# Optimization experiments

Hardware: AMD Instinct MI355X
Metric: run time of the kernel (lower is better)

## Reference

```python
import jax, jax.numpy as jnp
import numpy as np

TEMPERATURE = 0.07
BASE_TEMPERATURE = 0.07
L_MAX = 16  # max number of session labels per dialogue
NEG_INF = -1e30


def setup_inputs() -> dict:
    key = jax.random.key(0)
    k1, k2, k3 = jax.random.split(key, 3)
    B, T, H = 128, 1024, 256
    features = jax.random.normal(k1, (B, T, H), dtype=jnp.float32)
    dialogue_lengths = jax.random.randint(k2, (B,), 1, T + 1)
    labels = jax.random.randint(k3, (B, T), 0, L_MAX)
    return {"features": features, "dialogue_lengths": dialogue_lengths, "labels": labels}


def reference(features, dialogue_lengths, labels):
    B, T, H = features.shape
    valid = jnp.arange(T)[None, :] < dialogue_lengths[:, None]            # [B,T]
    # one-hot label assignment, zeroed at padded positions
    oh = (labels[..., None] == jnp.arange(L_MAX)[None, None, :]) & valid[..., None]
    ohf = oh.astype(features.dtype)                                       # [B,T,L]
    counts = ohf.sum(axis=1)                                              # [B,L]
    # per-dialogue, per-label prototype = mean of member features
    proto_sum = jnp.einsum('btl,bth->blh', ohf, features)                 # [B,L,H]
    prototypes = proto_sum / jnp.maximum(counts, 1.0)[..., None]          # [B,L,H]
    # anchor-vs-prototype logits
    logits = jnp.einsum('bth,blh->btl', features, prototypes) / TEMPERATURE
    present = counts > 0                                                  # [B,L]
    logits = jnp.where(present[:, None, :], logits, NEG_INF)
    log_prob = jax.nn.log_softmax(logits, axis=-1)                        # [B,T,L]
    # mask is one-hot on each token's own label -> mean_log_prob_pos is log_prob at own label
    pos = jnp.take_along_axis(log_prob, labels[..., None], axis=-1)[..., 0]  # [B,T]
    tok_loss = -(TEMPERATURE / BASE_TEMPERATURE) * pos
    per_dialogue = jnp.sum(jnp.where(valid, tok_loss, 0.0), axis=1) / dialogue_lengths.astype(features.dtype)
    return per_dialogue.mean()
```

## Files before the change

kernel.cpp:

```cpp
#include <hip/hip_runtime.h>
#include <math.h>

#define B 128
#define T 1024
#define H 256
#define L 16
#define INV_TEMP (1.0f/0.07f)
#define NEG_INF -1e30f


__global__ __launch_bounds__(256) void proto_kernel(
    const float* __restrict__ feat, const int* __restrict__ dlen,
    const int* __restrict__ labels, float* __restrict__ ws_pp,
    int* __restrict__ ws_cntp) {
  __shared__ float acc[4][L * 128];
  __shared__ int labs[256];
  __shared__ int cnt[L];

  const int bx = blockIdx.x;
  const int b = bx >> 3;
  const int chunk = (bx >> 2) & 1;
  const int seg = bx & 3;
  const int tid = threadIdx.x;
  const int w = tid >> 6;
  const int lane = tid & 63;

  const int len = dlen[b];
  if (seg * 256 >= len) return;

  for (int i = tid; i < 4 * L * 128; i += 256) ((float*)acc)[i] = 0.f;
  labs[tid] = labels[(size_t)b * T + seg * 256 + tid];
  if (tid < L) cnt[tid] = 0;
  __syncthreads();

  if (chunk == 0 && (seg * 256 + tid) < len) atomicAdd(&cnt[labs[tid]], 1);

  int nt = len - seg * 256 - w * 64;
  if (nt > 64) nt = 64;
  const float2* fbase = (const float2*)(feat +
      ((size_t)b * T + seg * 256 + w * 64) * H + chunk * 128);
  float* a = acc[w];

  int j = 0;
  for (; j + 4 <= nt; j += 4) {
    float2 f0 = fbase[(size_t)(j + 0) * (H / 2) + lane];
    float2 f1 = fbase[(size_t)(j + 1) * (H / 2) + lane];
    float2 f2 = fbase[(size_t)(j + 2) * (H / 2) + lane];
    float2 f3 = fbase[(size_t)(j + 3) * (H / 2) + lane];
    const int l0 = labs[w * 64 + j + 0];
    const int l1 = labs[w * 64 + j + 1];
    const int l2 = labs[w * 64 + j + 2];
    const int l3 = labs[w * 64 + j + 3];
    float2* p0 = (float2*)&a[l0 * 128 + lane * 2];
    { float2 v = *p0; v.x += f0.x; v.y += f0.y; *p0 = v; }
    float2* p1 = (float2*)&a[l1 * 128 + lane * 2];
    { float2 v = *p1; v.x += f1.x; v.y += f1.y; *p1 = v; }
    float2* p2 = (float2*)&a[l2 * 128 + lane * 2];
    { float2 v = *p2; v.x += f2.x; v.y += f2.y; *p2 = v; }
    float2* p3 = (float2*)&a[l3 * 128 + lane * 2];
    { float2 v = *p3; v.x += f3.x; v.y += f3.y; *p3 = v; }
  }
  for (; j < nt; ++j) {
    float2 f = fbase[(size_t)j * (H / 2) + lane];
    const int lab = labs[w * 64 + j];
    float2* p = (float2*)&a[lab * 128 + lane * 2];
    float2 v = *p; v.x += f.x; v.y += f.y; *p = v;
  }
  __syncthreads();

  float* op = ws_pp + (((size_t)b * 4 + seg) * L) * H + chunk * 128;
  for (int e = tid; e < L * 128; e += 256) {
    const float s = acc[0][e] + acc[1][e] + acc[2][e] + acc[3][e];
    op[(e >> 7) * H + (e & 127)] = s;
  }
  if (chunk == 0 && tid < L) ws_cntp[(b * 4 + seg) * L + tid] = cnt[tid];
}

__global__ __launch_bounds__(256) void dots_kernel(
    const float* __restrict__ feat, const int* __restrict__ dlen,
    const float* __restrict__ ws_pp, const int* __restrict__ ws_cntp,
    float* __restrict__ ws_dots) {
  __shared__ float pr[L * 128];
  __shared__ int cnts[L];

  const int bx = blockIdx.x;
  const int b = bx >> 1;
  const int half = bx & 1;
  const int tid = threadIdx.x;

  const int len = dlen[b];
  const int nseg = (len + 255) >> 8;

  if (tid < L) {
    const int* cp = ws_cntp + b * 4 * L + tid;
    int c = 0;
    for (int s = 0; s < nseg; ++s) c += cp[s * L];
    cnts[tid] = c;
  }
  __syncthreads();

  const float* gp = ws_pp + ((size_t)b * 4 * L) * H + half * 128;
  for (int i = tid; i < L * 128; i += 256) {
    const int l = i >> 7, c = i & 127;
    float s = 0.f;
    for (int sg = 0; sg < nseg; ++sg) s += gp[(sg * L + l) * H + c];
    const int cn = cnts[l];
    pr[i] = s * (cn > 0 ? 1.f / (float)cn : 0.f);
  }
  __syncthreads();

  const float4* fv[4];
#pragma unroll
  for (int k = 0; k < 4; ++k) {
    const int t = k * 256 + tid;
    fv[k] = (const float4*)(feat + ((size_t)b * T + t) * H + half * 128);
  }

  float dot[4][L];
#pragma unroll
  for (int k = 0; k < 4; ++k)
#pragma unroll
    for (int l = 0; l < L; ++l) dot[k][l] = 0.f;

  for (int cb = 0; cb < 8; ++cb) {
    float4 f[4][4];
#pragma unroll
    for (int k = 0; k < 4; ++k) {
      if (k < nseg) {
#pragma unroll
        for (int q = 0; q < 4; ++q) f[k][q] = fv[k][cb * 4 + q];
      }
    }
#pragma unroll
    for (int q = 0; q < 4; ++q) {
#pragma unroll
      for (int l = 0; l < L; ++l) {
        const float4 p = *(const float4*)&pr[l * 128 + cb * 16 + q * 4];
#pragma unroll
        for (int k = 0; k < 4; ++k) {
          if (k < nseg) {
            dot[k][l] += f[k][q].x * p.x + f[k][q].y * p.y +
                         f[k][q].z * p.z + f[k][q].w * p.w;
          }
        }
      }
    }
  }

#pragma unroll
  for (int k = 0; k < 4; ++k) {
    const int t = k * 256 + tid;
    if (k < nseg && t < len) {
      float4* d = (float4*)(ws_dots + (((size_t)half * B + b) * T + t) * L);
#pragma unroll
      for (int q = 0; q < 4; ++q)
        d[q] = make_float4(dot[k][q * 4], dot[k][q * 4 + 1],
                           dot[k][q * 4 + 2], dot[k][q * 4 + 3]);
    }
  }
}

__global__ __launch_bounds__(256) void loss_kernel(
    const int* __restrict__ dlen, const int* __restrict__ labels,
    const int* __restrict__ ws_cntp, const float* __restrict__ ws_dots,
    float* __restrict__ out) {
  __shared__ int cnts[L];
  __shared__ float red[256];

  const int b = blockIdx.x >> 2;
  const int seg = blockIdx.x & 3;
  const int tid = threadIdx.x;

  const int len = dlen[b];
  if (seg * 256 >= len) return;
  const int nseg = (len + 255) >> 8;

  if (tid < L) {
    const int* cp = ws_cntp + b * 4 * L + tid;
    int c = 0;
    for (int s = 0; s < nseg; ++s) c += cp[s * L];
    cnts[tid] = c;
  }
  __syncthreads();

  const int t = seg * 256 + tid;
  float tok = 0.f;

  if (t < len) {
    const float* d0 = ws_dots + ((size_t)b * T + t) * L;
    const float* d1 = d0 + (size_t)B * T * L;
    float lg[L];
#pragma unroll
    for (int l = 0; l < L; ++l) {
      const float d = d0[l] + d1[l];
      lg[l] = (cnts[l] > 0) ? d * INV_TEMP : NEG_INF;
    }
    float m = lg[0];
#pragma unroll
    for (int l = 1; l < L; ++l) m = fmaxf(m, lg[l]);
    float se = 0.f;
#pragma unroll
    for (int l = 0; l < L; ++l) se += expf(lg[l] - m);
    const float lsp = m + logf(se);

    const int lab = labels[(size_t)b * T + t];
    float pos = 0.f;
#pragma unroll
    for (int l = 0; l < L; ++l) pos += (l == lab) ? lg[l] : 0.f;

    tok = lsp - pos;
  }

  red[tid] = tok;
  __syncthreads();
#pragma unroll
  for (int s = 128; s > 0; s >>= 1) {
    if (tid < s) red[tid] += red[tid + s];
    __syncthreads();
  }
  if (tid == 0) atomicAdd(out, red[0] / ((float)len * (float)B));
}

extern "C" void kernel_launch(void* const* d_in, const int* in_sizes, int n_in,
                              void* d_out, int out_size, void* d_ws, size_t ws_size,
                              hipStream_t stream) {
  const float* feat = (const float*)d_in[0];
  const int* dlen = (const int*)d_in[1];
  const int* labels = (const int*)d_in[2];
  float* out = (float*)d_out;

  float* ws_pp = (float*)d_ws;
  int* ws_cntp = (int*)(ws_pp + (size_t)B * 4 * L * H);
  float* ws_dots = (float*)(ws_cntp + (size_t)B * 4 * L);

  hipMemsetAsync(out, 0, sizeof(float), stream);
  proto_kernel<<<B * 8, 256, 0, stream>>>(feat, dlen, labels, ws_pp, ws_cntp);
  dots_kernel<<<B * 2, 256, 0, stream>>>(feat, dlen, ws_pp, ws_cntp, ws_dots);
  loss_kernel<<<B * 4, 256, 0, stream>>>(dlen, labels, ws_cntp, ws_dots, out);
}
```

Baseline: 226.3 us.

## Fuse dot-product and loss kernels, split tokens instead of hidden dim

The dots and loss kernels become one. Each block now holds the full 256-wide prototype set in shared memory and owns up to 512 tokens, so every thread has complete logits and computes the log-softmax loss in registers. This drops the dots workspace round trip, the cross-half reduction and one launch. Blocks past the dialogue length exit early. In exchange each block stages twice as much prototype data, and per-thread work grows with full-H dot products.

```diff
diff --git a/kernel.cpp b/kernel.cpp
--- a/kernel.cpp
+++ b/kernel.cpp
@@ -76,19 +76,21 @@
   if (chunk == 0 && tid < L) ws_cntp[(b * 4 + seg) * L + tid] = cnt[tid];
 }
 
-__global__ __launch_bounds__(256) void dots_kernel(
+__global__ __launch_bounds__(256) void dots_loss_kernel(
     const float* __restrict__ feat, const int* __restrict__ dlen,
-    const float* __restrict__ ws_pp, const int* __restrict__ ws_cntp,
-    float* __restrict__ ws_dots) {
-  __shared__ float pr[L * 128];
+    const int* __restrict__ labels, const float* __restrict__ ws_pp,
+    const int* __restrict__ ws_cntp, float* __restrict__ out) {
+  __shared__ float pr[L * H];
   __shared__ int cnts[L];
+  __shared__ float red[256];
 
   const int bx = blockIdx.x;
   const int b = bx >> 1;
-  const int half = bx & 1;
+  const int g = bx & 1;
   const int tid = threadIdx.x;
 
   const int len = dlen[b];
+  if (g * 512 >= len) return;
   const int nseg = (len + 255) >> 8;
 
   if (tid < L) {
@@ -99,9 +101,9 @@
   }
   __syncthreads();
 
-  const float* gp = ws_pp + ((size_t)b * 4 * L) * H + half * 128;
-  for (int i = tid; i < L * 128; i += 256) {
-    const int l = i >> 7, c = i & 127;
+  const float* gp = ws_pp + ((size_t)b * 4 * L) * H;
+  for (int i = tid; i < L * H; i += 256) {
+    const int l = i >> 8, c = i & 255;
     float s = 0.f;
     for (int sg = 0; sg < nseg; ++sg) s += gp[(sg * L + l) * H + c];
     const int cn = cnts[l];
@@ -109,92 +111,43 @@
   }
   __syncthreads();
 
-  const float4* fv[4];
-#pragma unroll
-  for (int k = 0; k < 4; ++k) {
-    const int t = k * 256 + tid;
-    fv[k] = (const float4*)(feat + ((size_t)b * T + t) * H + half * 128);
-  }
-
-  float dot[4][L];
-#pragma unroll
-  for (int k = 0; k < 4; ++k)
-#pragma unroll
-    for (int l = 0; l < L; ++l) dot[k][l] = 0.f;
-
-  for (int cb = 0; cb < 8; ++cb) {
-    float4 f[4][4];
-#pragma unroll
-    for (int k = 0; k < 4; ++k) {
-      if (k < nseg) {
-#pragma unroll
-        for (int q = 0; q < 4; ++q) f[k][q] = fv[k][cb * 4 + q];
+  const int t0 = g * 512 + tid;
+  const int t1 = t0 + 256;
+  const bool v1 = (g * 512 + 256) < len;
+  const float4* fv0 = (const float4*)(feat + ((size_t)b * T + t0) * H);
+  const float4* fv1 = (const float4*)(feat + ((size_t)b * T + t1) * H);
+
+  float dot0[L], dot1[L];
+#pragma unroll
+  for (int l = 0; l < L; ++l) { dot0[l] = 0.f; dot1[l] = 0.f; }
+
+#pragma unroll 2
+  for (int cb = 0; cb < 16; ++cb) {
+    float4 f0[4], f1[4];
+#pragma unroll
+    for (int q = 0; q < 4; ++q) f0[q] = fv0[cb * 4 + q];
+    if (v1) {
+#pragma unroll
+      for (int q = 0; q < 4; ++q) f1[q] = fv1[cb * 4 + q];
+    }
+#pragma unroll
+    for (int q = 0; q < 4; ++q) {
+#pragma unroll
+      for (int l = 0; l < L; ++l) {
+        const float4 p = *(const float4*)&pr[l * H + cb * 16 + q * 4];
+        dot0[l] += f0[q].x * p.x + f0[q].y * p.y + f0[q].z * p.z + f0[q].w * p.w;
+        if (v1)
+          dot1[l] += f1[q].x * p.x + f1[q].y * p.y + f1[q].z * p.z + f1[q].w * p.w;
       }
     }
-#pragma unroll
-    for (int q = 0; q < 4; ++q) {
-#pragma unroll
-      for (int l = 0; l < L; ++l) {
-        const float4 p = *(const float4*)&pr[l * 128 + cb * 16 + q * 4];
-#pragma unroll
-        for (int k = 0; k < 4; ++k) {
-          if (k < nseg) {
-            dot[k][l] += f[k][q].x * p.x + f[k][q].y * p.y +
-                         f[k][q].z * p.z + f[k][q].w * p.w;
-          }
-        }
-      }
-    }
-  }
-
-#pragma unroll
-  for (int k = 0; k < 4; ++k) {
-    const int t = k * 256 + tid;
-    if (k < nseg && t < len) {
-      float4* d = (float4*)(ws_dots + (((size_t)half * B + b) * T + t) * L);
-#pragma unroll
-      for (int q = 0; q < 4; ++q)
-        d[q] = make_float4(dot[k][q * 4], dot[k][q * 4 + 1],
-                           dot[k][q * 4 + 2], dot[k][q * 4 + 3]);
-    }
-  }
-}
-
-__global__ __launch_bounds__(256) void loss_kernel(
-    const int* __restrict__ dlen, const int* __restrict__ labels,
-    const int* __restrict__ ws_cntp, const float* __restrict__ ws_dots,
-    float* __restrict__ out) {
-  __shared__ int cnts[L];
-  __shared__ float red[256];
-
-  const int b = blockIdx.x >> 2;
-  const int seg = blockIdx.x & 3;
-  const int tid = threadIdx.x;
-
-  const int len = dlen[b];
-  if (seg * 256 >= len) return;
-  const int nseg = (len + 255) >> 8;
-
-  if (tid < L) {
-    const int* cp = ws_cntp + b * 4 * L + tid;
-    int c = 0;
-    for (int s = 0; s < nseg; ++s) c += cp[s * L];
-    cnts[tid] = c;
-  }
-  __syncthreads();
-
-  const int t = seg * 256 + tid;
+  }
+
   float tok = 0.f;
-
-  if (t < len) {
-    const float* d0 = ws_dots + ((size_t)b * T + t) * L;
-    const float* d1 = d0 + (size_t)B * T * L;
+  if (t0 < len) {
     float lg[L];
 #pragma unroll
-    for (int l = 0; l < L; ++l) {
-      const float d = d0[l] + d1[l];
-      lg[l] = (cnts[l] > 0) ? d * INV_TEMP : NEG_INF;
-    }
+    for (int l = 0; l < L; ++l)
+      lg[l] = (cnts[l] > 0) ? dot0[l] * INV_TEMP : NEG_INF;
     float m = lg[0];
 #pragma unroll
     for (int l = 1; l < L; ++l) m = fmaxf(m, lg[l]);
@@ -202,13 +155,29 @@
 #pragma unroll
     for (int l = 0; l < L; ++l) se += expf(lg[l] - m);
     const float lsp = m + logf(se);
-
-    const int lab = labels[(size_t)b * T + t];
+    const int lab = labels[(size_t)b * T + t0];
     float pos = 0.f;
 #pragma unroll
     for (int l = 0; l < L; ++l) pos += (l == lab) ? lg[l] : 0.f;
-
-    tok = lsp - pos;
+    tok += lsp - pos;
+  }
+  if (v1 && t1 < len) {
+    float lg[L];
+#pragma unroll
+    for (int l = 0; l < L; ++l)
+      lg[l] = (cnts[l] > 0) ? dot1[l] * INV_TEMP : NEG_INF;
+    float m = lg[0];
+#pragma unroll
+    for (int l = 1; l < L; ++l) m = fmaxf(m, lg[l]);
+    float se = 0.f;
+#pragma unroll
+    for (int l = 0; l < L; ++l) se += expf(lg[l] - m);
+    const float lsp = m + logf(se);
+    const int lab = labels[(size_t)b * T + t1];
+    float pos = 0.f;
+#pragma unroll
+    for (int l = 0; l < L; ++l) pos += (l == lab) ? lg[l] : 0.f;
+    tok += lsp - pos;
   }
 
   red[tid] = tok;
@@ -231,10 +200,9 @@
 
   float* ws_pp = (float*)d_ws;
   int* ws_cntp = (int*)(ws_pp + (size_t)B * 4 * L * H);
-  float* ws_dots = (float*)(ws_cntp + (size_t)B * 4 * L);
 
   hipMemsetAsync(out, 0, sizeof(float), stream);
   proto_kernel<<<B * 8, 256, 0, stream>>>(feat, dlen, labels, ws_pp, ws_cntp);
-  dots_kernel<<<B * 2, 256, 0, stream>>>(feat, dlen, ws_pp, ws_cntp, ws_dots);
-  loss_kernel<<<B * 4, 256, 0, stream>>>(dlen, labels, ws_cntp, ws_dots, out);
+  dots_loss_kernel<<<B * 2, 256, 0, stream>>>(feat, dlen, labels, ws_pp,
+                                              ws_cntp, out);
 }
```

Result: slower. 241.9 us (+6.9%).
